# Kernel optimization log

Hardware: AMD Instinct MI355X
Metric: run time of the kernel (lower is better)

Reference implementation:

```python
import jax, jax.numpy as jnp
import numpy as np

N_GROUPS = 368
NMODELS = 64
BATCH = 4096


def setup_inputs() -> dict:
    key = jax.random.key(0)
    kx, kw, kb = jax.random.split(key, 3)
    x = jax.random.normal(kx, (BATCH, N_GROUPS, NMODELS), dtype=jnp.float32)
    # torch.nn.Linear default init: U(-1/sqrt(fan_in), 1/sqrt(fan_in))
    bound = 1.0 / np.sqrt(NMODELS)
    # W[i] is the [out, in] weight of the i-th Linear
    W = jax.random.uniform(kw, (N_GROUPS, NMODELS, NMODELS), dtype=jnp.float32, minval=-bound, maxval=bound)
    b = jax.random.uniform(kb, (N_GROUPS, NMODELS), dtype=jnp.float32, minval=-bound, maxval=bound)
    return {"x": x, "W": W, "b": b}


def reference(x, W, b):
    # y[b,g,:] = x[b,g,:] @ W[g].T + b[g]  -> grouped tiny GEMM, batched as one einsum
    y = jnp.einsum('bgn,gmn->bgm', x, W) + b[None, :, :]
    resp = jax.nn.softmax(y, axis=-1)  # softmax over feature axis per group
    # elementwise mul with x and reduce feature axis -> [B, 368]
    return (resp * x).sum(axis=-1)
```

## Files before the change

### kernel.cpp

```cpp
#include <hip/hip_runtime.h>
#include <hip/hip_fp16.h>
#include <stdint.h>

#define N_GROUPS 368
#define NMODELS  64
#define BATCH    4096
#define WAVES    8
#define ROWS_BLK 256

typedef __attribute__((ext_vector_type(8)))  _Float16 half8v;
typedef __attribute__((ext_vector_type(4)))  _Float16 half4v;
typedef __attribute__((ext_vector_type(16))) float    f32x16;

#define SWZ(row, soff) ((soff) ^ (((row) & 7) << 3))
#define XS(row, slot)  ((slot) ^ ((row) & 15))

__global__ __launch_bounds__(512, 4) void ensemble_dma(
    const float* __restrict__ x,
    const float* __restrict__ W,
    const float* __restrict__ bias,
    float* __restrict__ out)
{
    __shared__ float    Xs[WAVES][32 * 64];
    __shared__ _Float16 Wh[64 * 64];
    __shared__ _Float16 Wl[64 * 64];

    const int g    = blockIdx.y;
    const int row0 = blockIdx.x * ROWS_BLK;
    const int t    = threadIdx.x;
    const int lane = t & 63;
    const int wv   = t >> 6;

    {
        const int rloc = lane >> 4;
        const int p    = lane & 15;
        #pragma unroll
        for (int j = 0; j < 8; ++j) {
            const int r = 4 * j + rloc;
            const int q = XS(r, p);
            const float* gsrc =
                x + ((size_t)(row0 + wv * 32 + r) * N_GROUPS + g) * NMODELS + 4 * q;
            __builtin_amdgcn_global_load_lds(
                (const __attribute__((address_space(1))) void*)gsrc,
                (__attribute__((address_space(3))) void*)&Xs[wv][4 * j * 64],
                16, 0, 0);
        }
    }

    {
        const int m  = t >> 3;
        const int wc = (t & 7) * 8;
        const float* __restrict__ Wgp = W + ((size_t)g * 64 + m) * 64 + wc;
        const float4 v0 = *reinterpret_cast<const float4*>(Wgp);
        const float4 v1 = *reinterpret_cast<const float4*>(Wgp + 4);
        half4v h0, l0, h1, l1;
        h0[0]=(_Float16)v0.x; l0[0]=(_Float16)(v0.x-(float)h0[0]);
        h0[1]=(_Float16)v0.y; l0[1]=(_Float16)(v0.y-(float)h0[1]);
        h0[2]=(_Float16)v0.z; l0[2]=(_Float16)(v0.z-(float)h0[2]);
        h0[3]=(_Float16)v0.w; l0[3]=(_Float16)(v0.w-(float)h0[3]);
        h1[0]=(_Float16)v1.x; l1[0]=(_Float16)(v1.x-(float)h1[0]);
        h1[1]=(_Float16)v1.y; l1[1]=(_Float16)(v1.y-(float)h1[1]);
        h1[2]=(_Float16)v1.z; l1[2]=(_Float16)(v1.z-(float)h1[2]);
        h1[3]=(_Float16)v1.w; l1[3]=(_Float16)(v1.w-(float)h1[3]);
        const int s0 = m * 64 + SWZ(m, wc);
        const int s1 = m * 64 + SWZ(m, wc + 4);
        *reinterpret_cast<half4v*>(&Wh[s0]) = h0;
        *reinterpret_cast<half4v*>(&Wl[s0]) = l0;
        *reinterpret_cast<half4v*>(&Wh[s1]) = h1;
        *reinterpret_cast<half4v*>(&Wl[s1]) = l1;
    }
    __syncthreads();

    const int cl = lane & 31;
    const int h2 = lane >> 5;
    const float* __restrict__ slab = &Xs[wv][0];

    f32x16 acc0, acc1;
    #pragma unroll
    for (int r = 0; r < 16; ++r) { acc0[r] = 0.f; acc1[r] = 0.f; }

    #pragma unroll
    for (int ks = 0; ks < 4; ++ks) {
        const int e  = ks * 4 + 2 * h2;
        const float4 xa = *reinterpret_cast<const float4*>(&slab[cl * 64 + 4 * XS(cl, e)]);
        const float4 xb = *reinterpret_cast<const float4*>(&slab[cl * 64 + 4 * XS(cl, e + 1)]);
        half8v bh;
        bh[0]=(_Float16)xa.x; bh[1]=(_Float16)xa.y; bh[2]=(_Float16)xa.z; bh[3]=(_Float16)xa.w;
        bh[4]=(_Float16)xb.x; bh[5]=(_Float16)xb.y; bh[6]=(_Float16)xb.z; bh[7]=(_Float16)xb.w;

        const int ko = ks * 16 + 8 * h2;
        const int wo0 = cl * 64 + SWZ(cl, ko);
        const half8v ah0 = *reinterpret_cast<const half8v*>(&Wh[wo0]);
        const half8v al0 = *reinterpret_cast<const half8v*>(&Wl[wo0]);
        acc0 = __builtin_amdgcn_mfma_f32_32x32x16_f16(ah0, bh, acc0, 0, 0, 0);
        acc0 = __builtin_amdgcn_mfma_f32_32x32x16_f16(al0, bh, acc0, 0, 0, 0);

        const int wo1 = (32 + cl) * 64 + SWZ(32 + cl, ko);
        const half8v ah1 = *reinterpret_cast<const half8v*>(&Wh[wo1]);
        const half8v al1 = *reinterpret_cast<const half8v*>(&Wl[wo1]);
        acc1 = __builtin_amdgcn_mfma_f32_32x32x16_f16(ah1, bh, acc1, 0, 0, 0);
        acc1 = __builtin_amdgcn_mfma_f32_32x32x16_f16(al1, bh, acc1, 0, 0, 0);
    }

    float y[2][16];
    #pragma unroll
    for (int tt = 0; tt < 2; ++tt)
        #pragma unroll
        for (int rq = 0; rq < 4; ++rq) {
            const float4 bv = *reinterpret_cast<const float4*>(
                bias + (size_t)g * 64 + tt * 32 + 8 * rq + 4 * h2);
            const f32x16& a = tt ? acc1 : acc0;
            y[tt][4*rq+0] = a[4*rq+0] + bv.x;
            y[tt][4*rq+1] = a[4*rq+1] + bv.y;
            y[tt][4*rq+2] = a[4*rq+2] + bv.z;
            y[tt][4*rq+3] = a[4*rq+3] + bv.w;
        }

    float mx = y[0][0];
    #pragma unroll
    for (int r = 1; r < 16; ++r) mx = fmaxf(mx, y[0][r]);
    #pragma unroll
    for (int r = 0; r < 16; ++r) mx = fmaxf(mx, y[1][r]);
    mx = fmaxf(mx, __shfl_xor(mx, 32));

    float S = 0.f, P = 0.f;
    #pragma unroll
    for (int tt = 0; tt < 2; ++tt)
        #pragma unroll
        for (int rq = 0; rq < 4; ++rq) {
            const int q = tt * 8 + 2 * rq + h2;
            const float4 xv4 = *reinterpret_cast<const float4*>(
                &slab[cl * 64 + 4 * XS(cl, q)]);
            const float e0 = __expf(y[tt][4*rq+0] - mx);
            const float e1 = __expf(y[tt][4*rq+1] - mx);
            const float e2 = __expf(y[tt][4*rq+2] - mx);
            const float e3 = __expf(y[tt][4*rq+3] - mx);
            S += (e0 + e1) + (e2 + e3);
            P = __builtin_fmaf(e0, xv4.x, P);
            P = __builtin_fmaf(e1, xv4.y, P);
            P = __builtin_fmaf(e2, xv4.z, P);
            P = __builtin_fmaf(e3, xv4.w, P);
        }
    S += __shfl_xor(S, 32);
    P += __shfl_xor(P, 32);

    if (h2 == 0)
        out[(size_t)(row0 + wv * 32 + cl) * N_GROUPS + g] = P / S;
}

extern "C" void kernel_launch(void* const* d_in, const int* in_sizes, int n_in,
                              void* d_out, int out_size, void* d_ws, size_t ws_size,
                              hipStream_t stream) {
    const float* x  = (const float*)d_in[0];
    const float* W  = (const float*)d_in[1];
    const float* b  = (const float*)d_in[2];
    float* out = (float*)d_out;

    dim3 grid(BATCH / ROWS_BLK, N_GROUPS);
    dim3 block(512);
    ensemble_dma<<<grid, block, 0, stream>>>(x, W, b, out);
}
```

Before: 99.03 us.

## Double-buffer x tiles per wave with async LDS loads across four tiles

```diff
diff --git a/kernel.cpp b/kernel.cpp
--- a/kernel.cpp
+++ b/kernel.cpp
@@ -5,8 +5,9 @@
 #define N_GROUPS 368
 #define NMODELS  64
 #define BATCH    4096
-#define WAVES    8
-#define ROWS_BLK 256
+#define WAVES    4
+#define TPW      4
+#define ROWS_BLK (WAVES * TPW * 32)
 
 typedef __attribute__((ext_vector_type(8)))  _Float16 half8v;
 typedef __attribute__((ext_vector_type(4)))  _Float16 half4v;
@@ -15,13 +16,22 @@
 #define SWZ(row, soff) ((soff) ^ (((row) & 7) << 3))
 #define XS(row, slot)  ((slot) ^ ((row) & 15))
 
-__global__ __launch_bounds__(512, 4) void ensemble_dma(
+__device__ inline void wait_vm8() {
+    asm volatile("s_waitcnt vmcnt(8)" ::: "memory");
+    __builtin_amdgcn_sched_barrier(0);
+}
+__device__ inline void wait_vm0() {
+    asm volatile("s_waitcnt vmcnt(0)" ::: "memory");
+    __builtin_amdgcn_sched_barrier(0);
+}
+
+__global__ __launch_bounds__(256, 2) void ensemble_wavepipe(
     const float* __restrict__ x,
     const float* __restrict__ W,
     const float* __restrict__ bias,
     float* __restrict__ out)
 {
-    __shared__ float    Xs[WAVES][32 * 64];
+    __shared__ float    Xs[WAVES][2][32 * 64];
     __shared__ _Float16 Wh[64 * 64];
     __shared__ _Float16 Wl[64 * 64];
 
@@ -31,121 +41,143 @@
     const int lane = t & 63;
     const int wv   = t >> 6;
 
+    const int rloc = lane >> 4;
+    const int p    = lane & 15;
+    const float* __restrict__ xw =
+        x + ((size_t)(row0 + wv * (TPW * 32)) * N_GROUPS + g) * NMODELS;
+    const size_t rowstep = (size_t)N_GROUPS * NMODELS;
+
+    #pragma unroll
+    for (int j = 0; j < 8; ++j) {
+        const int r = 4 * j + rloc;
+        const int q = XS(r, p);
+        __builtin_amdgcn_global_load_lds(
+            (const __attribute__((address_space(1))) void*)(xw + (size_t)r * rowstep + 4 * q),
+            (__attribute__((address_space(3))) void*)&Xs[wv][0][4 * j * 64],
+            16, 0, 0);
+    }
+
     {
-        const int rloc = lane >> 4;
-        const int p    = lane & 15;
+        const int m  = t >> 2;
+        const int wc = (t & 3) * 16;
+        const float* __restrict__ Wgp = W + ((size_t)g * 64 + m) * 64 + wc;
         #pragma unroll
-        for (int j = 0; j < 8; ++j) {
-            const int r = 4 * j + rloc;
-            const int q = XS(r, p);
-            const float* gsrc =
-                x + ((size_t)(row0 + wv * 32 + r) * N_GROUPS + g) * NMODELS + 4 * q;
-            __builtin_amdgcn_global_load_lds(
-                (const __attribute__((address_space(1))) void*)gsrc,
-                (__attribute__((address_space(3))) void*)&Xs[wv][4 * j * 64],
-                16, 0, 0);
+        for (int j = 0; j < 4; ++j) {
+            const float4 v = *reinterpret_cast<const float4*>(Wgp + 4 * j);
+            half4v h, l;
+            h[0]=(_Float16)v.x; l[0]=(_Float16)(v.x-(float)h[0]);
+            h[1]=(_Float16)v.y; l[1]=(_Float16)(v.y-(float)h[1]);
+            h[2]=(_Float16)v.z; l[2]=(_Float16)(v.z-(float)h[2]);
+            h[3]=(_Float16)v.w; l[3]=(_Float16)(v.w-(float)h[3]);
+            const int so = m * 64 + SWZ(m, wc + 4 * j);
+            *reinterpret_cast<half4v*>(&Wh[so]) = h;
+            *reinterpret_cast<half4v*>(&Wl[so]) = l;
         }
     }
 
-    {
-        const int m  = t >> 3;
-        const int wc = (t & 7) * 8;
-        const float* __restrict__ Wgp = W + ((size_t)g * 64 + m) * 64 + wc;
-        const float4 v0 = *reinterpret_cast<const float4*>(Wgp);
-        const float4 v1 = *reinterpret_cast<const float4*>(Wgp + 4);
-        half4v h0, l0, h1, l1;
-        h0[0]=(_Float16)v0.x; l0[0]=(_Float16)(v0.x-(float)h0[0]);
-        h0[1]=(_Float16)v0.y; l0[1]=(_Float16)(v0.y-(float)h0[1]);
-        h0[2]=(_Float16)v0.z; l0[2]=(_Float16)(v0.z-(float)h0[2]);
-        h0[3]=(_Float16)v0.w; l0[3]=(_Float16)(v0.w-(float)h0[3]);
-        h1[0]=(_Float16)v1.x; l1[0]=(_Float16)(v1.x-(float)h1[0]);
-        h1[1]=(_Float16)v1.y; l1[1]=(_Float16)(v1.y-(float)h1[1]);
-        h1[2]=(_Float16)v1.z; l1[2]=(_Float16)(v1.z-(float)h1[2]);
-        h1[3]=(_Float16)v1.w; l1[3]=(_Float16)(v1.w-(float)h1[3]);
-        const int s0 = m * 64 + SWZ(m, wc);
-        const int s1 = m * 64 + SWZ(m, wc + 4);
-        *reinterpret_cast<half4v*>(&Wh[s0]) = h0;
-        *reinterpret_cast<half4v*>(&Wl[s0]) = l0;
-        *reinterpret_cast<half4v*>(&Wh[s1]) = h1;
-        *reinterpret_cast<half4v*>(&Wl[s1]) = l1;
-    }
-    __syncthreads();
-
     const int cl = lane & 31;
     const int h2 = lane >> 5;
-    const float* __restrict__ slab = &Xs[wv][0];
 
-    f32x16 acc0, acc1;
-    #pragma unroll
-    for (int r = 0; r < 16; ++r) { acc0[r] = 0.f; acc1[r] = 0.f; }
-
-    #pragma unroll
-    for (int ks = 0; ks < 4; ++ks) {
-        const int e  = ks * 4 + 2 * h2;
-        const float4 xa = *reinterpret_cast<const float4*>(&slab[cl * 64 + 4 * XS(cl, e)]);
-        const float4 xb = *reinterpret_cast<const float4*>(&slab[cl * 64 + 4 * XS(cl, e + 1)]);
-        half8v bh;
-        bh[0]=(_Float16)xa.x; bh[1]=(_Float16)xa.y; bh[2]=(_Float16)xa.z; bh[3]=(_Float16)xa.w;
-        bh[4]=(_Float16)xb.x; bh[5]=(_Float16)xb.y; bh[6]=(_Float16)xb.z; bh[7]=(_Float16)xb.w;
-
-        const int ko = ks * 16 + 8 * h2;
-        const int wo0 = cl * 64 + SWZ(cl, ko);
-        const half8v ah0 = *reinterpret_cast<const half8v*>(&Wh[wo0]);
-        const half8v al0 = *reinterpret_cast<const half8v*>(&Wl[wo0]);
-        acc0 = __builtin_amdgcn_mfma_f32_32x32x16_f16(ah0, bh, acc0, 0, 0, 0);
-        acc0 = __builtin_amdgcn_mfma_f32_32x32x16_f16(al0, bh, acc0, 0, 0, 0);
-
-        const int wo1 = (32 + cl) * 64 + SWZ(32 + cl, ko);
-        const half8v ah1 = *reinterpret_cast<const half8v*>(&Wh[wo1]);
-        const half8v al1 = *reinterpret_cast<const half8v*>(&Wl[wo1]);
-        acc1 = __builtin_amdgcn_mfma_f32_32x32x16_f16(ah1, bh, acc1, 0, 0, 0);
-        acc1 = __builtin_amdgcn_mfma_f32_32x32x16_f16(al1, bh, acc1, 0, 0, 0);
-    }
-
-    float y[2][16];
+    float4 bv4[2][4];
     #pragma unroll
     for (int tt = 0; tt < 2; ++tt)
         #pragma unroll
-        for (int rq = 0; rq < 4; ++rq) {
-            const float4 bv = *reinterpret_cast<const float4*>(
+        for (int rq = 0; rq < 4; ++rq)
+            bv4[tt][rq] = *reinterpret_cast<const float4*>(
                 bias + (size_t)g * 64 + tt * 32 + 8 * rq + 4 * h2);
-            const f32x16& a = tt ? acc1 : acc0;
-            y[tt][4*rq+0] = a[4*rq+0] + bv.x;
-            y[tt][4*rq+1] = a[4*rq+1] + bv.y;
-            y[tt][4*rq+2] = a[4*rq+2] + bv.z;
-            y[tt][4*rq+3] = a[4*rq+3] + bv.w;
+
+    __syncthreads();
+
+    #pragma unroll
+    for (int tile = 0; tile < TPW; ++tile) {
+        if (tile + 1 < TPW) {
+            const float* __restrict__ xt = xw + (size_t)(tile + 1) * 32 * rowstep;
+            #pragma unroll
+            for (int j = 0; j < 8; ++j) {
+                const int r = 4 * j + rloc;
+                const int q = XS(r, p);
+                __builtin_amdgcn_global_load_lds(
+                    (const __attribute__((address_space(1))) void*)(xt + (size_t)r * rowstep + 4 * q),
+                    (__attribute__((address_space(3))) void*)&Xs[wv][(tile + 1) & 1][4 * j * 64],
+                    16, 0, 0);
+            }
+            wait_vm8();
+        } else {
+            wait_vm0();
         }
 
-    float mx = y[0][0];
-    #pragma unroll
-    for (int r = 1; r < 16; ++r) mx = fmaxf(mx, y[0][r]);
-    #pragma unroll
-    for (int r = 0; r < 16; ++r) mx = fmaxf(mx, y[1][r]);
-    mx = fmaxf(mx, __shfl_xor(mx, 32));
+        const float* __restrict__ slab = &Xs[wv][tile & 1][0];
 
-    float S = 0.f, P = 0.f;
-    #pragma unroll
-    for (int tt = 0; tt < 2; ++tt)
+        f32x16 acc0, acc1;
         #pragma unroll
-        for (int rq = 0; rq < 4; ++rq) {
-            const int q = tt * 8 + 2 * rq + h2;
-            const float4 xv4 = *reinterpret_cast<const float4*>(
-                &slab[cl * 64 + 4 * XS(cl, q)]);
-            const float e0 = __expf(y[tt][4*rq+0] - mx);
-            const float e1 = __expf(y[tt][4*rq+1] - mx);
-            const float e2 = __expf(y[tt][4*rq+2] - mx);
-            const float e3 = __expf(y[tt][4*rq+3] - mx);
-            S += (e0 + e1) + (e2 + e3);
-            P = __builtin_fmaf(e0, xv4.x, P);
-            P = __builtin_fmaf(e1, xv4.y, P);
-            P = __builtin_fmaf(e2, xv4.z, P);
-            P = __builtin_fmaf(e3, xv4.w, P);
+        for (int r = 0; r < 16; ++r) { acc0[r] = 0.f; acc1[r] = 0.f; }
+
+        #pragma unroll
+        for (int ks = 0; ks < 4; ++ks) {
+            const int e  = ks * 4 + 2 * h2;
+            const float4 xa = *reinterpret_cast<const float4*>(&slab[cl * 64 + 4 * XS(cl, e)]);
+            const float4 xb = *reinterpret_cast<const float4*>(&slab[cl * 64 + 4 * XS(cl, e + 1)]);
+            half8v bh;
+            bh[0]=(_Float16)xa.x; bh[1]=(_Float16)xa.y; bh[2]=(_Float16)xa.z; bh[3]=(_Float16)xa.w;
+            bh[4]=(_Float16)xb.x; bh[5]=(_Float16)xb.y; bh[6]=(_Float16)xb.z; bh[7]=(_Float16)xb.w;
+
+            const int ko = ks * 16 + 8 * h2;
+            const int wo0 = cl * 64 + SWZ(cl, ko);
+            const half8v ah0 = *reinterpret_cast<const half8v*>(&Wh[wo0]);
+            const half8v al0 = *reinterpret_cast<const half8v*>(&Wl[wo0]);
+            acc0 = __builtin_amdgcn_mfma_f32_32x32x16_f16(ah0, bh, acc0, 0, 0, 0);
+            acc0 = __builtin_amdgcn_mfma_f32_32x32x16_f16(al0, bh, acc0, 0, 0, 0);
+
+            const int wo1 = (32 + cl) * 64 + SWZ(32 + cl, ko);
+            const half8v ah1 = *reinterpret_cast<const half8v*>(&Wh[wo1]);
+            const half8v al1 = *reinterpret_cast<const half8v*>(&Wl[wo1]);
+            acc1 = __builtin_amdgcn_mfma_f32_32x32x16_f16(ah1, bh, acc1, 0, 0, 0);
+            acc1 = __builtin_amdgcn_mfma_f32_32x32x16_f16(al1, bh, acc1, 0, 0, 0);
         }
-    S += __shfl_xor(S, 32);
-    P += __shfl_xor(P, 32);
 
-    if (h2 == 0)
-        out[(size_t)(row0 + wv * 32 + cl) * N_GROUPS + g] = P / S;
+        float y[2][16];
+        #pragma unroll
+        for (int tt = 0; tt < 2; ++tt)
+            #pragma unroll
+            for (int rq = 0; rq < 4; ++rq) {
+                const f32x16& a = tt ? acc1 : acc0;
+                y[tt][4*rq+0] = a[4*rq+0] + bv4[tt][rq].x;
+                y[tt][4*rq+1] = a[4*rq+1] + bv4[tt][rq].y;
+                y[tt][4*rq+2] = a[4*rq+2] + bv4[tt][rq].z;
+                y[tt][4*rq+3] = a[4*rq+3] + bv4[tt][rq].w;
+            }
+
+        float mx = y[0][0];
+        #pragma unroll
+        for (int r = 1; r < 16; ++r) mx = fmaxf(mx, y[0][r]);
+        #pragma unroll
+        for (int r = 0; r < 16; ++r) mx = fmaxf(mx, y[1][r]);
+        mx = fmaxf(mx, __shfl_xor(mx, 32));
+
+        float S = 0.f, P = 0.f;
+        #pragma unroll
+        for (int tt = 0; tt < 2; ++tt)
+            #pragma unroll
+            for (int rq = 0; rq < 4; ++rq) {
+                const int q = tt * 8 + 2 * rq + h2;
+                const float4 xv4 = *reinterpret_cast<const float4*>(
+                    &slab[cl * 64 + 4 * XS(cl, q)]);
+                const float e0 = __expf(y[tt][4*rq+0] - mx);
+                const float e1 = __expf(y[tt][4*rq+1] - mx);
+                const float e2 = __expf(y[tt][4*rq+2] - mx);
+                const float e3 = __expf(y[tt][4*rq+3] - mx);
+                S += (e0 + e1) + (e2 + e3);
+                P = __builtin_fmaf(e0, xv4.x, P);
+                P = __builtin_fmaf(e1, xv4.y, P);
+                P = __builtin_fmaf(e2, xv4.z, P);
+                P = __builtin_fmaf(e3, xv4.w, P);
+            }
+        S += __shfl_xor(S, 32);
+        P += __shfl_xor(P, 32);
+
+        if (h2 == 0)
+            out[(size_t)(row0 + wv * (TPW * 32) + tile * 32 + cl) * N_GROUPS + g] = P / S;
+    }
 }
 
 extern "C" void kernel_launch(void* const* d_in, const int* in_sizes, int n_in,
@@ -157,6 +189,6 @@
     float* out = (float*)d_out;
 
     dim3 grid(BATCH / ROWS_BLK, N_GROUPS);
-    dim3 block(512);
-    ensemble_dma<<<grid, block, 0, stream>>>(x, W, b, out);
+    dim3 block(WAVES * 64);
+    ensemble_wavepipe<<<grid, block, 0, stream>>>(x, W, b, out);
 }
```

Result: slower. 101.4 us (+2.4%).
